# Performance work log

Hardware: AMD Instinct MI355X
Metric: run time of the kernel (lower is better)

## Reference

```python
import jax, jax.numpy as jnp
import numpy as np

L, B, H, D, S, FF = 24, 4, 16, 512, 4096, 2048
HD = D // H
POS = 2048  # current kv_cache_len (write position)
EPS = 1e-5
SCALE = 1.0 / np.sqrt(HD)


def layer_norm(x, w, b):
    m = jnp.mean(x, axis=-1, keepdims=True)
    v = jnp.mean(jnp.square(x - m), axis=-1, keepdims=True)
    return (x - m) * jax.lax.rsqrt(v + EPS) * w + b


def setup_inputs() -> dict:
    key = jax.random.key(0)
    ks = jax.random.split(key, 12)
    f = lambda k, shape: jax.random.normal(k, shape, dtype=jnp.float32) * 0.02
    # decode mask: positions [0, POS] are attendable (index_fill_ sets POS True)
    attn_mask = jnp.broadcast_to(jnp.arange(S) <= POS, (B, H, 1, S))
    return {
        "x": jax.random.normal(ks[0], (B, 1, D), dtype=jnp.float32),
        "k_cache": jax.random.normal(ks[1], (L, B, H, S, HD), dtype=jnp.float32),
        "v_cache": jax.random.normal(ks[2], (L, B, H, S, HD), dtype=jnp.float32),
        "attn_mask": attn_mask,
        "qkv_w": f(ks[3], (L, 3 * D, D)),
        "qkv_b": f(ks[4], (L, 3 * D)),
        "out_w": f(ks[5], (L, D, D)),
        "out_b": f(ks[6], (L, D)),
        "mlp_w1": f(ks[7], (L, FF, D)),
        "mlp_b1": f(ks[8], (L, FF)),
        "mlp_w2": f(ks[9], (L, D, FF)),
        "mlp_b2": f(ks[10], (L, D)),
        "norm_w1": jnp.ones((L, D), jnp.float32),
        "norm_b1": jnp.zeros((L, D), jnp.float32),
        "norm_w2": jnp.ones((L, D), jnp.float32),
        "norm_b2": jnp.zeros((L, D), jnp.float32),
        "kv_cache_len": POS,
    }


def reference(x, k_cache, v_cache, attn_mask, qkv_w, qkv_b, out_w, out_b,
              mlp_w1, mlp_b1, mlp_w2, mlp_b2, norm_w1, norm_b1, norm_w2,
              norm_b2, kv_cache_len):
    pos = kv_cache_len

    def block(h, p):
        kc0, vc0, qw, qb, ow, ob, w1, b1, w2, b2, nw1, nb1, nw2, nb2 = p
        qkv = h @ qw.T + qb                      # [B,1,3D]
        q, k, v = jnp.split(qkv, 3, axis=-1)
        q = q.reshape(B, 1, H, HD).transpose(0, 2, 1, 3)   # [B,H,1,HD]
        k = k.reshape(B, 1, H, HD).transpose(0, 2, 1, 3)
        v = v.reshape(B, 1, H, HD).transpose(0, 2, 1, 3)
        # in-place cache update at write position (index_copy_ on dim 2)
        kc = kc0.at[:, :, pos, :].set(k[:, :, 0, :])       # [B,H,S,HD]
        vc = vc0.at[:, :, pos, :].set(v[:, :, 0, :])
        scores = jnp.einsum('bhqd,bhkd->bhqk', q, kc) * SCALE
        scores = jnp.where(attn_mask, scores, -1e9)
        attn = jnp.einsum('bhqk,bhkd->bhqd', jax.nn.softmax(scores, axis=-1), vc)
        attn = attn.transpose(0, 2, 1, 3).reshape(B, 1, D)
        attn = attn @ ow.T + ob
        h = layer_norm(h + attn, nw1, nb1)
        mlp = jax.nn.relu(h @ w1.T + b1) @ w2.T + b2
        h = layer_norm(h + mlp, nw2, nb2)
        return h, None

    xs = (k_cache, v_cache, qkv_w, qkv_b, out_w, out_b, mlp_w1, mlp_b1,
          mlp_w2, mlp_b2, norm_w1, norm_b1, norm_w2, norm_b2)
    out, _ = jax.lax.scan(block, x, xs)
    return out
```

## Files before the change

### kernel.cpp

```cpp
#include <hip/hip_runtime.h>
#include <hip/hip_cooperative_groups.h>

namespace cg = cooperative_groups;


#define DEV __device__ __forceinline__

static constexpr int LNUM = 24;
static constexpr int B = 4;
static constexpr int H = 16;
static constexpr int D = 512;
static constexpr int S = 4096;
static constexpr int FF = 2048;
static constexpr int HD = 32;
static constexpr int NCH = 9;
static constexpr float EPS = 1e-5f;
static constexpr float SCALE = 0.17677669529663687f;

DEV float waveReduceSum(float v) {
#pragma unroll
    for (int o = 32; o > 0; o >>= 1) v += __shfl_xor(v, o);
    return v;
}
DEV float waveReduceMax(float v) {
#pragma unroll
    for (int o = 32; o > 0; o >>= 1) v = fmaxf(v, __shfl_xor(v, o));
    return v;
}
DEV float blockReduceSum(float v, volatile float* red) {
    v = waveReduceSum(v);
    __syncthreads();
    if ((threadIdx.x & 63) == 0) red[threadIdx.x >> 6] = v;
    __syncthreads();
    return red[0] + red[1] + red[2] + red[3];
}
DEV float blockReduceMax(float v, volatile float* red) {
    v = waveReduceMax(v);
    __syncthreads();
    if ((threadIdx.x & 63) == 0) red[threadIdx.x >> 6] = v;
    __syncthreads();
    return fmaxf(fmaxf(red[0], red[1]), fmaxf(red[2], red[3]));
}

struct Params {
    const float *x, *kc, *vc;
    const float *qkvw, *qkvb, *outw, *outb, *w1, *b1, *w2, *b2;
    const float *nw1, *nb1, *nw2, *nb2;
    const int* posp;
    float *qkvbuf, *part, *t1, *m1, *sbuf, *out;
};

__global__ __launch_bounds__(256, 2) void mega(Params p) {
    cg::grid_group grid = cg::this_grid();
    const int blk = blockIdx.x;
    const int tid = threadIdx.x;
    const int w = tid >> 6;
    const int lane = tid & 63;
    const int pos = p.posp[0];

    __shared__ float SM[6160];
    float* red = SM + 6152;

    for (int l = 0; l < LNUM; ++l) {
        const float* hsrc = (l == 0) ? p.x : p.sbuf;
        const bool aln = (l > 0);
        const float* pnw = p.nw2 + (aln ? (size_t)(l - 1) * 512 : 0);
        const float* pnb = p.nb2 + (aln ? (size_t)(l - 1) * 512 : 0);
        const float* qwL = p.qkvw + (size_t)l * 1536 * 512;
        const float* qbL = p.qkvb + (size_t)l * 1536;
        const float* kcL = p.kc + (size_t)l * 8388608;
        const float* vcL = p.vc + (size_t)l * 8388608;
        const float* owL = p.outw + (size_t)l * 512 * 512;
        const float* obL = p.outb + (size_t)l * 512;
        const float* w1L = p.w1 + (size_t)l * 2048 * 512;
        const float* b1L = p.b1 + (size_t)l * 2048;
        const float* w2L = p.w2 + (size_t)l * 512 * 2048;
        const float* b2L = p.b2 + (size_t)l * 512;
        const float* n1w = p.nw1 + (size_t)l * 512;
        const float* n1b = p.nb1 + (size_t)l * 512;

        {
            const float4* s4 = (const float4*)hsrc;
            float4* m4 = (float4*)SM;
            m4[tid] = s4[tid];
            m4[tid + 256] = s4[tid + 256];
            __syncthreads();
            float4* h4 = (float4*)(SM + (w << 9));
            float4 aa = h4[lane], bb = h4[lane + 64];
            float s = aa.x + aa.y + aa.z + aa.w + bb.x + bb.y + bb.z + bb.w;
            float s2 = aa.x * aa.x + aa.y * aa.y + aa.z * aa.z + aa.w * aa.w
                     + bb.x * bb.x + bb.y * bb.y + bb.z * bb.z + bb.w * bb.w;
            s = waveReduceSum(s);
            s2 = waveReduceSum(s2);
            float mean = s * (1.f / 512.f);
            float rs = rsqrtf(s2 * (1.f / 512.f) - mean * mean + EPS);
            if (aln) {
                const float4* gw4 = (const float4*)pnw;
                const float4* gb4 = (const float4*)pnb;
                float4 gw = gw4[lane], gb = gb4[lane];
                aa.x = (aa.x - mean) * rs * gw.x + gb.x;
                aa.y = (aa.y - mean) * rs * gw.y + gb.y;
                aa.z = (aa.z - mean) * rs * gw.z + gb.z;
                aa.w = (aa.w - mean) * rs * gw.w + gb.w;
                h4[lane] = aa;
                gw = gw4[lane + 64]; gb = gb4[lane + 64];
                bb.x = (bb.x - mean) * rs * gw.x + gb.x;
                bb.y = (bb.y - mean) * rs * gw.y + gb.y;
                bb.z = (bb.z - mean) * rs * gw.z + gb.z;
                bb.w = (bb.w - mean) * rs * gw.w + gb.w;
                h4[lane + 64] = bb;
            }
            __syncthreads();
            const int r = (blk << 2) + w;
            if (r < 1536) {
                const float4* wr4 = (const float4*)(qwL + (size_t)r * 512);
                float4 wA = wr4[lane], wB = wr4[lane + 64];
                float acc[4];
#pragma unroll
                for (int b = 0; b < 4; ++b) {
                    const float4* hb4 = (const float4*)(SM + (b << 9));
                    float4 hA = hb4[lane], hB = hb4[lane + 64];
                    float a = wA.x * hA.x + wA.y * hA.y + wA.z * hA.z + wA.w * hA.w
                            + wB.x * hB.x + wB.y * hB.y + wB.z * hB.z + wB.w * hB.w;
                    acc[b] = waveReduceSum(a);
                }
                if (lane == 0) {
                    float bias = qbL[r];
                    float sc = (r < 512) ? SCALE : 1.f;
#pragma unroll
                    for (int b = 0; b < 4; ++b)
                        p.qkvbuf[b * 1536 + r] = (acc[b] + bias) * sc;
                }
            }
        }
        grid.sync();

        {
            const int c = blk & 7, bh = blk >> 3;
            const int b = bh >> 4, h = bh & 15;
            float* qs = SM;
            float* es = SM + 32;
            float* op = SM + 288;
            float* sn = SM + 560;
            if (tid < 32) qs[tid] = p.qkvbuf[b * 1536 + h * 32 + tid];
            __syncthreads();
            const int pp = (c << 8) + tid;
            const bool act = pp < pos;
            const float4* kp = (const float4*)(kcL + ((size_t)bh * 4096 + pp) * 32);
            float sc = 0.f;
#pragma unroll
            for (int i = 0; i < 8; ++i) {
                float4 kv = kp[i];
                sc += qs[4 * i] * kv.x + qs[4 * i + 1] * kv.y
                    + qs[4 * i + 2] * kv.z + qs[4 * i + 3] * kv.w;
            }
            float score = act ? sc : -1e30f;
            float smax = score;
            float snew = 0.f;
            if (c == 7 && tid == 0) {
                const float* kn = p.qkvbuf + b * 1536 + 512 + h * 32;
                for (int j = 0; j < 32; ++j) snew += qs[j] * kn[j];
                smax = fmaxf(smax, snew);
            }
            float m = blockReduceMax(smax, red);
            if (tid == 0) sn[0] = (c == 7) ? expf(snew - m) : 0.f;
            float e = act ? expf(score - m) : 0.f;
            es[tid] = e;
            float lsum = blockReduceSum(e, red) + sn[0];
            const int d = tid & 31, g = tid >> 5;
            float acc = 0.f;
            const float* vp = vcL + ((size_t)bh * 4096 + (c << 8) + (g << 5)) * 32 + d;
#pragma unroll 8
            for (int i = 0; i < 32; ++i) acc += es[(g << 5) + i] * vp[(size_t)i * 32];
            if (g == 0) acc += sn[0] * p.qkvbuf[b * 1536 + 1024 + h * 32 + d];
            op[g * 33 + d] = acc;
            __syncthreads();
            if (tid < 32) {
                float o = 0.f;
#pragma unroll
                for (int gg = 0; gg < 8; ++gg) o += op[gg * 33 + tid];
                float* pt = p.part + (size_t)((bh << 3) + c) * 34;
                pt[2 + tid] = o;
                if (tid == 0) { pt[0] = m; pt[1] = lsum; }
            }
        }
        grid.sync();

        {
            const float4* s4 = (const float4*)hsrc;
            float4* m4 = (float4*)SM;
            m4[tid] = s4[tid];
            m4[tid + 256] = s4[tid + 256];
            __syncthreads();
            float4* h4 = (float4*)(SM + (w << 9));
            float4 aa = h4[lane], bb = h4[lane + 64];
            float s = aa.x + aa.y + aa.z + aa.w + bb.x + bb.y + bb.z + bb.w;
            float s2 = aa.x * aa.x + aa.y * aa.y + aa.z * aa.z + aa.w * aa.w
                     + bb.x * bb.x + bb.y * bb.y + bb.z * bb.z + bb.w * bb.w;
            s = waveReduceSum(s);
            s2 = waveReduceSum(s2);
            float mean = s * (1.f / 512.f);
            float rs = rsqrtf(s2 * (1.f / 512.f) - mean * mean + EPS);
            if (tid < 64) {
                const float* pt = p.part + (size_t)(tid << 3) * 34;
                float mh = -1e30f;
#pragma unroll
                for (int cc = 0; cc < 8; ++cc) mh = fmaxf(mh, pt[cc * 34]);
                float ssum = 0.f;
#pragma unroll
                for (int cc = 0; cc < 8; ++cc) ssum += pt[cc * 34 + 1] * expf(pt[cc * 34] - mh);
                SM[2048 + tid] = mh;
                SM[2112 + tid] = ssum;
            }
            __syncthreads();
#pragma unroll
            for (int k = 0; k < 8; ++k) {
                int idx = tid + (k << 8);
                int b = idx >> 9, e = idx & 511, hh = e >> 5, dd = e & 31;
                int bh = (b << 4) + hh;
                const float* pt = p.part + (size_t)(bh << 3) * 34;
                float mh = SM[2048 + bh];
                float inv = 1.f / SM[2112 + bh];
                float o = 0.f;
#pragma unroll
                for (int cc = 0; cc < 8; ++cc) o += pt[cc * 34 + 2 + dd] * expf(pt[cc * 34] - mh);
                SM[2176 + idx] = o * inv;
            }
            __syncthreads();
            const int dd = blk;
            const float4* wr4 = (const float4*)(owL + (size_t)dd * 512);
            float4 wA = wr4[lane], wB = wr4[lane + 64];
            const float4* a4 = (const float4*)(SM + 2176 + (w << 9));
            float4 hA = a4[lane], hB = a4[lane + 64];
            float acc = wA.x * hA.x + wA.y * hA.y + wA.z * hA.z + wA.w * hA.w
                      + wB.x * hB.x + wB.y * hB.y + wB.z * hB.z + wB.w * hB.w;
            acc = waveReduceSum(acc);
            if (lane == 0) {
                float hv = SM[(w << 9) + dd];
                if (aln) hv = (hv - mean) * rs * pnw[dd] + pnb[dd];
                p.t1[(w << 9) + dd] = hv + acc + obL[dd];
            }
        }
        grid.sync();

        {
            const float4* s4 = (const float4*)p.t1;
            float4* m4 = (float4*)SM;
            m4[tid] = s4[tid];
            m4[tid + 256] = s4[tid + 256];
            __syncthreads();
            float4* h4 = (float4*)(SM + (w << 9));
            float4 aa = h4[lane], bb = h4[lane + 64];
            float s = aa.x + aa.y + aa.z + aa.w + bb.x + bb.y + bb.z + bb.w;
            float s2 = aa.x * aa.x + aa.y * aa.y + aa.z * aa.z + aa.w * aa.w
                     + bb.x * bb.x + bb.y * bb.y + bb.z * bb.z + bb.w * bb.w;
            s = waveReduceSum(s);
            s2 = waveReduceSum(s2);
            float mean = s * (1.f / 512.f);
            float rs = rsqrtf(s2 * (1.f / 512.f) - mean * mean + EPS);
            {
                const float4* gw4 = (const float4*)n1w;
                const float4* gb4 = (const float4*)n1b;
                float4 gw = gw4[lane], gb = gb4[lane];
                aa.x = (aa.x - mean) * rs * gw.x + gb.x;
                aa.y = (aa.y - mean) * rs * gw.y + gb.y;
                aa.z = (aa.z - mean) * rs * gw.z + gb.z;
                aa.w = (aa.w - mean) * rs * gw.w + gb.w;
                h4[lane] = aa;
                gw = gw4[lane + 64]; gb = gb4[lane + 64];
                bb.x = (bb.x - mean) * rs * gw.x + gb.x;
                bb.y = (bb.y - mean) * rs * gw.y + gb.y;
                bb.z = (bb.z - mean) * rs * gw.z + gb.z;
                bb.w = (bb.w - mean) * rs * gw.w + gb.w;
                h4[lane + 64] = bb;
            }
            __syncthreads();
            const int r = (blk << 2) + w;
            const float4* wr4 = (const float4*)(w1L + (size_t)r * 512);
            float4 wA = wr4[lane], wB = wr4[lane + 64];
            float acc[4];
#pragma unroll
            for (int b = 0; b < 4; ++b) {
                const float4* hb4 = (const float4*)(SM + (b << 9));
                float4 hA = hb4[lane], hB = hb4[lane + 64];
                float a = wA.x * hA.x + wA.y * hA.y + wA.z * hA.z + wA.w * hA.w
                        + wB.x * hB.x + wB.y * hB.y + wB.z * hB.z + wB.w * hB.w;
                acc[b] = waveReduceSum(a);
            }
            if (lane == 0) {
                float bv = b1L[r];
#pragma unroll
                for (int b = 0; b < 4; ++b)
                    p.m1[(b << 11) + r] = fmaxf(acc[b] + bv, 0.f);
            }
        }
        grid.sync();

        {
            const float4* t4 = (const float4*)p.t1;
            float4* tB = (float4*)(SM + 4096);
            tB[tid] = t4[tid];
            tB[tid + 256] = t4[tid + 256];
            __syncthreads();
            const float4* h4 = (const float4*)(SM + 4096 + (w << 9));
            float4 aa = h4[lane], bb = h4[lane + 64];
            float s = aa.x + aa.y + aa.z + aa.w + bb.x + bb.y + bb.z + bb.w;
            float s2 = aa.x * aa.x + aa.y * aa.y + aa.z * aa.z + aa.w * aa.w
                     + bb.x * bb.x + bb.y * bb.y + bb.z * bb.z + bb.w * bb.w;
            s = waveReduceSum(s);
            s2 = waveReduceSum(s2);
            float mean = s * (1.f / 512.f);
            float rs = rsqrtf(s2 * (1.f / 512.f) - mean * mean + EPS);
            const int dd = blk;
            const float4* wr4 = (const float4*)(w2L + (size_t)dd * 2048);
            float acc = 0.f;
#pragma unroll
            for (int half = 0; half < 2; ++half) {
                __syncthreads();
#pragma unroll
                for (int i = 0; i < 4; ++i) {
                    int idx = tid + (i << 8);
                    int b = idx >> 8;
                    int f = idx & 255;
                    ((float4*)SM)[idx] =
                        ((const float4*)(p.m1 + (b << 11) + (half << 10)))[f];
                }
                __syncthreads();
                const float4* mb4 = (const float4*)SM + (w << 8);
#pragma unroll
                for (int i = 0; i < 4; ++i) {
                    float4 q = wr4[(half << 8) + (i << 6) + lane];
                    float4 mm = mb4[(i << 6) + lane];
                    acc += q.x * mm.x + q.y * mm.y + q.z * mm.z + q.w * mm.w;
                }
            }
            acc = waveReduceSum(acc);
            if (lane == 0) {
                float tv = SM[4096 + (w << 9) + dd];
                float hv = (tv - mean) * rs * n1w[dd] + n1b[dd];
                p.sbuf[(w << 9) + dd] = hv + acc + b2L[dd];
            }
        }
        grid.sync();
    }

    if (blk < 4) {
        const int b = blk;
        const float* nw = p.nw2 + 23 * 512;
        const float* nb = p.nb2 + 23 * 512;
        float a0 = p.sbuf[(b << 9) + tid];
        float a1 = p.sbuf[(b << 9) + 256 + tid];
        float s = blockReduceSum(a0 + a1, red);
        float s2 = blockReduceSum(a0 * a0 + a1 * a1, red);
        float mean = s * (1.f / 512.f);
        float rs = rsqrtf(s2 * (1.f / 512.f) - mean * mean + EPS);
        p.out[(b << 9) + tid] = (a0 - mean) * rs * nw[tid] + nb[tid];
        p.out[(b << 9) + 256 + tid] = (a1 - mean) * rs * nw[tid + 256] + nb[tid + 256];
    }
}

__global__ __launch_bounds__(256) void k_qkv(
    const float* __restrict__ hsrc, int apply_ln,
    const float* __restrict__ nw, const float* __restrict__ nb,
    const float* __restrict__ w, const float* __restrict__ bias,
    float* __restrict__ qkv)
{
    const int lane = threadIdx.x & 63;
    const int wid = (blockIdx.x << 2) + (threadIdx.x >> 6);
    const int b = wid / 1536;
    const int r = wid - b * 1536;
    const float* hb = hsrc + (b << 9);
    const int k0 = lane << 3;
    float4 h0 = *(const float4*)(hb + k0);
    float4 h1 = *(const float4*)(hb + k0 + 4);
    float hv[8] = {h0.x, h0.y, h0.z, h0.w, h1.x, h1.y, h1.z, h1.w};
    if (apply_ln) {
        float s = 0.f, s2 = 0.f;
#pragma unroll
        for (int j = 0; j < 8; ++j) { s += hv[j]; s2 += hv[j] * hv[j]; }
        s = waveReduceSum(s);
        s2 = waveReduceSum(s2);
        float mean = s * (1.f / 512.f);
        float rs = rsqrtf(s2 * (1.f / 512.f) - mean * mean + EPS);
        float4 nw0 = *(const float4*)(nw + k0);
        float4 nw1 = *(const float4*)(nw + k0 + 4);
        float4 nb0 = *(const float4*)(nb + k0);
        float4 nb1 = *(const float4*)(nb + k0 + 4);
        float nwv[8] = {nw0.x, nw0.y, nw0.z, nw0.w, nw1.x, nw1.y, nw1.z, nw1.w};
        float nbv[8] = {nb0.x, nb0.y, nb0.z, nb0.w, nb1.x, nb1.y, nb1.z, nb1.w};
#pragma unroll
        for (int j = 0; j < 8; ++j) hv[j] = (hv[j] - mean) * rs * nwv[j] + nbv[j];
    }
    const float* wr = w + (size_t)r * 512 + k0;
    float4 w0 = *(const float4*)(wr);
    float4 w1 = *(const float4*)(wr + 4);
    float acc = w0.x * hv[0] + w0.y * hv[1] + w0.z * hv[2] + w0.w * hv[3]
              + w1.x * hv[4] + w1.y * hv[5] + w1.z * hv[6] + w1.w * hv[7];
    acc = waveReduceSum(acc);
    if (lane == 0) {
        float v = acc + bias[r];
        if (r < 512) v *= SCALE;
        qkv[b * 1536 + r] = v;
    }
}

__global__ __launch_bounds__(256) void k_attn(
    const float* __restrict__ kc, const float* __restrict__ vc,
    const float* __restrict__ qkv, float* __restrict__ part,
    const int* __restrict__ posp)
{
    const int tid = threadIdx.x;
    const int c = blockIdx.x % NCH;
    const int bh = blockIdx.x / NCH;
    const int b = bh >> 4, h = bh & 15;
    const int pos = posp[0];
    __shared__ float qs[32];
    __shared__ float es[256];
    __shared__ float red[4];
    __shared__ float op[8][33];
    if (tid < 32) qs[tid] = qkv[b * 1536 + h * 32 + tid];
    __syncthreads();
    float score = -1e30f;
    bool act = false;
    if (c < 8) {
        int p = c * 256 + tid;
        act = (p < pos);
        const float4* kp = (const float4*)(kc + ((size_t)bh * S + p) * HD);
        float s = 0.f;
#pragma unroll
        for (int i = 0; i < 8; ++i) {
            float4 kv = kp[i];
            s += qs[4 * i] * kv.x + qs[4 * i + 1] * kv.y + qs[4 * i + 2] * kv.z + qs[4 * i + 3] * kv.w;
        }
        if (act) score = s;
    } else if (tid == 0) {
        act = true;
        const float* kp = qkv + b * 1536 + 512 + h * 32;
        float s = 0.f;
#pragma unroll
        for (int j = 0; j < 32; ++j) s += qs[j] * kp[j];
        score = s;
    }
    float m = blockReduceMax(score, red);
    float e = act ? expf(score - m) : 0.f;
    es[tid] = e;
    float l = blockReduceSum(e, red);
    const int d = tid & 31, g = tid >> 5;
    float acc = 0.f;
    if (c < 8) {
        const float* vp = vc + ((size_t)bh * S + c * 256 + g * 32) * HD + d;
#pragma unroll 8
        for (int i = 0; i < 32; ++i) acc += es[g * 32 + i] * vp[(size_t)i * HD];
    } else if (g == 0) {
        acc = es[0] * qkv[b * 1536 + 1024 + h * 32 + d];
    }
    op[g][d] = acc;
    __syncthreads();
    if (tid < 32) {
        float o = 0.f;
#pragma unroll
        for (int gg = 0; gg < 8; ++gg) o += op[gg][tid];
        float* pp = part + (size_t)(bh * NCH + c) * 34;
        pp[2 + tid] = o;
        if (tid == 0) { pp[0] = m; pp[1] = l; }
    }
}

__global__ __launch_bounds__(256) void k_outproj(
    const float* __restrict__ part,
    const float* __restrict__ ow, const float* __restrict__ ob,
    const float* __restrict__ hsrc, int apply_ln,
    const float* __restrict__ nw, const float* __restrict__ nb,
    float* __restrict__ t1)
{
    const int tid = threadIdx.x;
    const int b = blockIdx.x >> 5;
    const int oc = blockIdx.x & 31;
    __shared__ float attn_s[512];
    __shared__ float hln[512];
    __shared__ float mh[16], sh[16];
    __shared__ float red[4];
    if (tid < 16) {
        const float* pp = part + (size_t)(b * 16 + tid) * NCH * 34;
        float m = -1e30f;
        for (int c = 0; c < NCH; ++c) m = fmaxf(m, pp[c * 34]);
        float ss = 0.f;
        for (int c = 0; c < NCH; ++c) ss += pp[c * 34 + 1] * expf(pp[c * 34] - m);
        mh[tid] = m;
        sh[tid] = ss;
    }
    __syncthreads();
#pragma unroll
    for (int e = tid; e < 512; e += 256) {
        int h = e >> 5, d = e & 31;
        const float* pp = part + (size_t)(b * 16 + h) * NCH * 34;
        float o = 0.f;
        for (int c = 0; c < NCH; ++c) o += pp[c * 34 + 2 + d] * expf(pp[c * 34] - mh[h]);
        attn_s[e] = o / sh[h];
    }
    float a0 = hsrc[(b << 9) + tid], a1 = hsrc[(b << 9) + 256 + tid];
    if (apply_ln) {
        float s = blockReduceSum(a0 + a1, red);
        float s2 = blockReduceSum(a0 * a0 + a1 * a1, red);
        float mean = s * (1.f / 512.f);
        float rs = rsqrtf(s2 * (1.f / 512.f) - mean * mean + EPS);
        hln[tid] = (a0 - mean) * rs * nw[tid] + nb[tid];
        hln[tid + 256] = (a1 - mean) * rs * nw[tid + 256] + nb[tid + 256];
    } else {
        hln[tid] = a0;
        hln[tid + 256] = a1;
    }
    __syncthreads();
    const int w = tid >> 6, lane = tid & 63, k0 = lane << 3;
#pragma unroll
    for (int oi = 0; oi < 4; ++oi) {
        int dd = (oc << 4) + (w << 2) + oi;
        const float4* wp = (const float4*)(ow + (size_t)dd * 512 + k0);
        float4 w0 = wp[0], w1 = wp[1];
        float acc = w0.x * attn_s[k0] + w0.y * attn_s[k0 + 1] + w0.z * attn_s[k0 + 2] + w0.w * attn_s[k0 + 3]
                  + w1.x * attn_s[k0 + 4] + w1.y * attn_s[k0 + 5] + w1.z * attn_s[k0 + 6] + w1.w * attn_s[k0 + 7];
        acc = waveReduceSum(acc);
        if (lane == 0) t1[(b << 9) + dd] = hln[dd] + acc + ob[dd];
    }
}

__global__ __launch_bounds__(256) void k_mlp1(
    const float* __restrict__ t1,
    const float* __restrict__ nw, const float* __restrict__ nb,
    const float* __restrict__ w1, const float* __restrict__ b1,
    float* __restrict__ m1)
{
    const int tid = threadIdx.x;
    const int b = blockIdx.x >> 7;
    const int oc = blockIdx.x & 127;
    __shared__ float hln[512];
    __shared__ float red[4];
    float a0 = t1[(b << 9) + tid], a1 = t1[(b << 9) + 256 + tid];
    float s = blockReduceSum(a0 + a1, red);
    float s2 = blockReduceSum(a0 * a0 + a1 * a1, red);
    float mean = s * (1.f / 512.f);
    float rs = rsqrtf(s2 * (1.f / 512.f) - mean * mean + EPS);
    hln[tid] = (a0 - mean) * rs * nw[tid] + nb[tid];
    hln[tid + 256] = (a1 - mean) * rs * nw[tid + 256] + nb[tid + 256];
    __syncthreads();
    const int w = tid >> 6, lane = tid & 63, k0 = lane << 3;
#pragma unroll
    for (int oi = 0; oi < 4; ++oi) {
        int r = (oc << 4) + (w << 2) + oi;
        const float4* wp = (const float4*)(w1 + (size_t)r * 512 + k0);
        float4 w0 = wp[0], w1v = wp[1];
        float acc = w0.x * hln[k0] + w0.y * hln[k0 + 1] + w0.z * hln[k0 + 2] + w0.w * hln[k0 + 3]
                  + w1v.x * hln[k0 + 4] + w1v.y * hln[k0 + 5] + w1v.z * hln[k0 + 6] + w1v.w * hln[k0 + 7];
        acc = waveReduceSum(acc);
        if (lane == 0) m1[(b << 11) + r] = fmaxf(acc + b1[r], 0.f);
    }
}

__global__ __launch_bounds__(256) void k_mlp2(
    const float* __restrict__ m1, const float* __restrict__ t1,
    const float* __restrict__ nw, const float* __restrict__ nb,
    const float* __restrict__ w2, const float* __restrict__ b2,
    float* __restrict__ sout)
{
    const int tid = threadIdx.x;
    const int b = blockIdx.x >> 7;
    const int oc = blockIdx.x & 127;
    __shared__ float ms[2048];
    __shared__ float red[4];
#pragma unroll
    for (int i = 0; i < 8; ++i) ms[tid + (i << 8)] = m1[(b << 11) + tid + (i << 8)];
    float a0 = t1[(b << 9) + tid], a1 = t1[(b << 9) + 256 + tid];
    float s = blockReduceSum(a0 + a1, red);
    float s2 = blockReduceSum(a0 * a0 + a1 * a1, red);
    float mean = s * (1.f / 512.f);
    float rs = rsqrtf(s2 * (1.f / 512.f) - mean * mean + EPS);
    const int w = tid >> 6, lane = tid & 63;
    const int dd = (oc << 2) + w;
    const float4* wp = (const float4*)(w2 + (size_t)dd * 2048);
    float acc = 0.f;
#pragma unroll
    for (int i = 0; i < 8; ++i) {
        int idx = (i << 6) + lane;
        float4 q = wp[idx];
        int k = idx << 2;
        acc += q.x * ms[k] + q.y * ms[k + 1] + q.z * ms[k + 2] + q.w * ms[k + 3];
    }
    acc = waveReduceSum(acc);
    if (lane == 0) {
        float td = t1[(b << 9) + dd];
        float hd = (td - mean) * rs * nw[dd] + nb[dd];
        sout[(b << 9) + dd] = hd + acc + b2[dd];
    }
}

__global__ __launch_bounds__(256) void k_finalln(
    const float* __restrict__ sbuf,
    const float* __restrict__ nw, const float* __restrict__ nb,
    float* __restrict__ out)
{
    const int b = blockIdx.x, tid = threadIdx.x;
    __shared__ float red[4];
    float a0 = sbuf[(b << 9) + tid], a1 = sbuf[(b << 9) + 256 + tid];
    float s = blockReduceSum(a0 + a1, red);
    float s2 = blockReduceSum(a0 * a0 + a1 * a1, red);
    float mean = s * (1.f / 512.f);
    float rs = rsqrtf(s2 * (1.f / 512.f) - mean * mean + EPS);
    out[(b << 9) + tid] = (a0 - mean) * rs * nw[tid] + nb[tid];
    out[(b << 9) + 256 + tid] = (a1 - mean) * rs * nw[tid + 256] + nb[tid + 256];
}

extern "C" void kernel_launch(void* const* d_in, const int* in_sizes, int n_in,
                              void* d_out, int out_size, void* d_ws, size_t ws_size,
                              hipStream_t stream)
{
    const float* x    = (const float*)d_in[0];
    const float* kc   = (const float*)d_in[1];
    const float* vc   = (const float*)d_in[2];
    const float* qkvw = (const float*)d_in[4];
    const float* qkvb = (const float*)d_in[5];
    const float* outw = (const float*)d_in[6];
    const float* outb = (const float*)d_in[7];
    const float* w1   = (const float*)d_in[8];
    const float* b1   = (const float*)d_in[9];
    const float* w2   = (const float*)d_in[10];
    const float* b2   = (const float*)d_in[11];
    const float* nw1  = (const float*)d_in[12];
    const float* nb1  = (const float*)d_in[13];
    const float* nw2  = (const float*)d_in[14];
    const float* nb2  = (const float*)d_in[15];
    const int*   posp = (const int*)d_in[16];

    int dev = 0, cu = 0, nb = 0;
    hipGetDevice(&dev);
    hipDeviceGetAttribute(&cu, hipDeviceAttributeMultiprocessorCount, dev);
    hipOccupancyMaxActiveBlocksPerMultiprocessor(&nb, (const void*)mega, 256, 0);
    const bool coop_ok = ((long)nb * cu >= 512);

    float* ws = (float*)d_ws;

    if (coop_ok) {
        Params prm;
        prm.x = x; prm.kc = kc; prm.vc = vc;
        prm.qkvw = qkvw; prm.qkvb = qkvb; prm.outw = outw; prm.outb = outb;
        prm.w1 = w1; prm.b1 = b1; prm.w2 = w2; prm.b2 = b2;
        prm.nw1 = nw1; prm.nb1 = nb1; prm.nw2 = nw2; prm.nb2 = nb2;
        prm.posp = posp;
        prm.qkvbuf = ws;
        prm.part   = prm.qkvbuf + 6144;
        prm.t1     = prm.part + 17408;
        prm.m1     = prm.t1 + 2048;
        prm.sbuf   = prm.m1 + 8192;
        prm.out    = (float*)d_out;
        void* args[] = { &prm };
        hipLaunchCooperativeKernel(reinterpret_cast<const void*>(&mega),
                                   dim3(512), dim3(256), args, 0, stream);
        return;
    }

    float* qkvbuf = ws;
    float* part   = qkvbuf + 6144;
    float* t1     = part + 19584;
    float* m1     = t1 + 2048;
    float* sbuf   = m1 + 8192;
    const size_t kvLayerStride = (size_t)B * H * S * HD;

    for (int l = 0; l < LNUM; ++l) {
        const float* hsrc = (l == 0) ? x : sbuf;
        const int aln = (l > 0) ? 1 : 0;
        const float* pnw = (l > 0) ? (nw2 + (size_t)(l - 1) * 512) : nullptr;
        const float* pnb = (l > 0) ? (nb2 + (size_t)(l - 1) * 512) : nullptr;

        k_qkv<<<1536, 256, 0, stream>>>(hsrc, aln, pnw, pnb,
                                        qkvw + (size_t)l * 1536 * 512,
                                        qkvb + (size_t)l * 1536, qkvbuf);
        k_attn<<<B * H * NCH, 256, 0, stream>>>(kc + (size_t)l * kvLayerStride,
                                                vc + (size_t)l * kvLayerStride,
                                                qkvbuf, part, posp);
        k_outproj<<<B * 32, 256, 0, stream>>>(part,
                                              outw + (size_t)l * 512 * 512,
                                              outb + (size_t)l * 512,
                                              hsrc, aln, pnw, pnb, t1);
        k_mlp1<<<B * 128, 256, 0, stream>>>(t1,
                                            nw1 + (size_t)l * 512, nb1 + (size_t)l * 512,
                                            w1 + (size_t)l * FF * D, b1 + (size_t)l * FF, m1);
        k_mlp2<<<B * 128, 256, 0, stream>>>(m1, t1,
                                            nw1 + (size_t)l * 512, nb1 + (size_t)l * 512,
                                            w2 + (size_t)l * D * FF, b2 + (size_t)l * 512, sbuf);
    }
    k_finalln<<<B, 256, 0, stream>>>(sbuf, nw2 + 23 * 512, nb2 + 23 * 512, (float*)d_out);
}
```

Measured before the change: 844.5 us.

## Replace grid.sync with split arrive/wait atomic barrier and prefetch weights before waits

Swaps the cooperative-groups grid sync for a monotonic atomic counter barrier split into an arrive phase and a wait phase. Each stage now loads the data that does not depend on the previous stage (K/V cache rows, out-proj, W1 and W2 rows, next layer's QKV rows, LN params) before waiting, so those global loads overlap barrier latency. This raises register pressure, since for example 32 V values and 8 W2 float4s are held per thread, and it relies on hand-written acquire/release fencing being correct. A memset of the counter is added before each launch.

```diff
diff --git a/kernel.cpp b/kernel.cpp
--- a/kernel.cpp
+++ b/kernel.cpp
@@ -1,7 +1,4 @@
 #include <hip/hip_runtime.h>
-#include <hip/hip_cooperative_groups.h>
-
-namespace cg = cooperative_groups;
 
 
 #define DEV __device__ __forceinline__
@@ -14,6 +11,7 @@
 static constexpr int FF = 2048;
 static constexpr int HD = 32;
 static constexpr int NCH = 9;
+static constexpr int NBLK = 512;
 static constexpr float EPS = 1e-5f;
 static constexpr float SCALE = 0.17677669529663687f;
 
@@ -40,6 +38,20 @@
     if ((threadIdx.x & 63) == 0) red[threadIdx.x >> 6] = v;
     __syncthreads();
     return fmaxf(fmaxf(red[0], red[1]), fmaxf(red[2], red[3]));
+}
+
+DEV void gbar_arrive(unsigned* ctr) {
+    __syncthreads();
+    if (threadIdx.x == 0)
+        __hip_atomic_fetch_add(ctr, 1u, __ATOMIC_RELEASE, __HIP_MEMORY_SCOPE_AGENT);
+}
+DEV void gbar_wait(unsigned* ctr, unsigned target) {
+    if (threadIdx.x == 0) {
+        while (__hip_atomic_load(ctr, __ATOMIC_RELAXED, __HIP_MEMORY_SCOPE_AGENT) < target)
+            __builtin_amdgcn_s_sleep(1);
+        __builtin_amdgcn_fence(__ATOMIC_ACQUIRE, "agent");
+    }
+    __syncthreads();
 }
 
 struct Params {
@@ -48,25 +60,34 @@
     const float *nw1, *nb1, *nw2, *nb2;
     const int* posp;
     float *qkvbuf, *part, *t1, *m1, *sbuf, *out;
+    unsigned* bar;
 };
 
 __global__ __launch_bounds__(256, 2) void mega(Params p) {
-    cg::grid_group grid = cg::this_grid();
     const int blk = blockIdx.x;
     const int tid = threadIdx.x;
     const int w = tid >> 6;
     const int lane = tid & 63;
     const int pos = p.posp[0];
+    unsigned* ctr = p.bar;
+    unsigned nbar = 0;
 
     __shared__ float SM[6160];
     float* red = SM + 6152;
+
+    const int r1 = (blk << 2) + w;
+
+    float4 wA, wB;
+    if (r1 < 1536) {
+        const float4* wr4 = (const float4*)(p.qkvw + (size_t)r1 * 512);
+        wA = wr4[lane]; wB = wr4[lane + 64];
+    }
 
     for (int l = 0; l < LNUM; ++l) {
         const float* hsrc = (l == 0) ? p.x : p.sbuf;
         const bool aln = (l > 0);
         const float* pnw = p.nw2 + (aln ? (size_t)(l - 1) * 512 : 0);
         const float* pnb = p.nb2 + (aln ? (size_t)(l - 1) * 512 : 0);
-        const float* qwL = p.qkvw + (size_t)l * 1536 * 512;
         const float* qbL = p.qkvb + (size_t)l * 1536;
         const float* kcL = p.kc + (size_t)l * 8388608;
         const float* vcL = p.vc + (size_t)l * 8388608;
@@ -80,16 +101,17 @@
         const float* n1b = p.nb1 + (size_t)l * 512;
 
         {
+            if (l) gbar_wait(ctr, nbar * NBLK);
             const float4* s4 = (const float4*)hsrc;
+            float4 hr0 = s4[tid], hr1 = s4[tid + 256];
             float4* m4 = (float4*)SM;
-            m4[tid] = s4[tid];
-            m4[tid + 256] = s4[tid + 256];
+            m4[tid] = hr0; m4[tid + 256] = hr1;
             __syncthreads();
             float4* h4 = (float4*)(SM + (w << 9));
-            float4 aa = h4[lane], bb = h4[lane + 64];
-            float s = aa.x + aa.y + aa.z + aa.w + bb.x + bb.y + bb.z + bb.w;
+            float4 aa = h4[lane], bbv = h4[lane + 64];
+            float s = aa.x + aa.y + aa.z + aa.w + bbv.x + bbv.y + bbv.z + bbv.w;
             float s2 = aa.x * aa.x + aa.y * aa.y + aa.z * aa.z + aa.w * aa.w
-                     + bb.x * bb.x + bb.y * bb.y + bb.z * bb.z + bb.w * bb.w;
+                     + bbv.x * bbv.x + bbv.y * bbv.y + bbv.z * bbv.z + bbv.w * bbv.w;
             s = waveReduceSum(s);
             s2 = waveReduceSum(s2);
             float mean = s * (1.f / 512.f);
@@ -104,17 +126,14 @@
                 aa.w = (aa.w - mean) * rs * gw.w + gb.w;
                 h4[lane] = aa;
                 gw = gw4[lane + 64]; gb = gb4[lane + 64];
-                bb.x = (bb.x - mean) * rs * gw.x + gb.x;
-                bb.y = (bb.y - mean) * rs * gw.y + gb.y;
-                bb.z = (bb.z - mean) * rs * gw.z + gb.z;
-                bb.w = (bb.w - mean) * rs * gw.w + gb.w;
-                h4[lane + 64] = bb;
-            }
-            __syncthreads();
-            const int r = (blk << 2) + w;
-            if (r < 1536) {
-                const float4* wr4 = (const float4*)(qwL + (size_t)r * 512);
-                float4 wA = wr4[lane], wB = wr4[lane + 64];
+                bbv.x = (bbv.x - mean) * rs * gw.x + gb.x;
+                bbv.y = (bbv.y - mean) * rs * gw.y + gb.y;
+                bbv.z = (bbv.z - mean) * rs * gw.z + gb.z;
+                bbv.w = (bbv.w - mean) * rs * gw.w + gb.w;
+                h4[lane + 64] = bbv;
+            }
+            __syncthreads();
+            if (r1 < 1536) {
                 float acc[4];
 #pragma unroll
                 for (int b = 0; b < 4; ++b) {
@@ -125,40 +144,49 @@
                     acc[b] = waveReduceSum(a);
                 }
                 if (lane == 0) {
-                    float bias = qbL[r];
-                    float sc = (r < 512) ? SCALE : 1.f;
+                    float bias = qbL[r1];
+                    float sc = (r1 < 512) ? SCALE : 1.f;
 #pragma unroll
                     for (int b = 0; b < 4; ++b)
-                        p.qkvbuf[b * 1536 + r] = (acc[b] + bias) * sc;
+                        p.qkvbuf[b * 1536 + r1] = (acc[b] + bias) * sc;
                 }
             }
+            gbar_arrive(ctr); ++nbar;
         }
-        grid.sync();
 
         {
             const int c = blk & 7, bh = blk >> 3;
-            const int b = bh >> 4, h = bh & 15;
+            const int bb2 = bh >> 4, hh2 = bh & 15;
+            const int pp2 = (c << 8) + tid;
+            float4 kpre[8];
+            {
+                const float4* kp = (const float4*)(kcL + ((size_t)bh * 4096 + pp2) * 32);
+#pragma unroll
+                for (int i = 0; i < 8; ++i) kpre[i] = kp[i];
+            }
+            float vpre[32];
+            {
+                const float* vp = vcL + ((size_t)bh * 4096 + (c << 8) + ((tid >> 5) << 5)) * 32 + (tid & 31);
+#pragma unroll
+                for (int i = 0; i < 32; ++i) vpre[i] = vp[(size_t)i * 32];
+            }
+            gbar_wait(ctr, nbar * NBLK);
             float* qs = SM;
             float* es = SM + 32;
             float* op = SM + 288;
             float* sn = SM + 560;
-            if (tid < 32) qs[tid] = p.qkvbuf[b * 1536 + h * 32 + tid];
-            __syncthreads();
-            const int pp = (c << 8) + tid;
-            const bool act = pp < pos;
-            const float4* kp = (const float4*)(kcL + ((size_t)bh * 4096 + pp) * 32);
+            if (tid < 32) qs[tid] = p.qkvbuf[bb2 * 1536 + (hh2 << 5) + tid];
+            __syncthreads();
             float sc = 0.f;
 #pragma unroll
-            for (int i = 0; i < 8; ++i) {
-                float4 kv = kp[i];
-                sc += qs[4 * i] * kv.x + qs[4 * i + 1] * kv.y
-                    + qs[4 * i + 2] * kv.z + qs[4 * i + 3] * kv.w;
-            }
+            for (int i = 0; i < 8; ++i)
+                sc += qs[4 * i] * kpre[i].x + qs[4 * i + 1] * kpre[i].y
+                    + qs[4 * i + 2] * kpre[i].z + qs[4 * i + 3] * kpre[i].w;
+            const bool act = pp2 < pos;
             float score = act ? sc : -1e30f;
-            float smax = score;
-            float snew = 0.f;
+            float smax = score, snew = 0.f;
             if (c == 7 && tid == 0) {
-                const float* kn = p.qkvbuf + b * 1536 + 512 + h * 32;
+                const float* kn = p.qkvbuf + bb2 * 1536 + 512 + (hh2 << 5);
                 for (int j = 0; j < 32; ++j) snew += qs[j] * kn[j];
                 smax = fmaxf(smax, snew);
             }
@@ -169,10 +197,9 @@
             float lsum = blockReduceSum(e, red) + sn[0];
             const int d = tid & 31, g = tid >> 5;
             float acc = 0.f;
-            const float* vp = vcL + ((size_t)bh * 4096 + (c << 8) + (g << 5)) * 32 + d;
-#pragma unroll 8
-            for (int i = 0; i < 32; ++i) acc += es[(g << 5) + i] * vp[(size_t)i * 32];
-            if (g == 0) acc += sn[0] * p.qkvbuf[b * 1536 + 1024 + h * 32 + d];
+#pragma unroll
+            for (int i = 0; i < 32; ++i) acc += es[(g << 5) + i] * vpre[i];
+            if (g == 0) acc += sn[0] * p.qkvbuf[bb2 * 1536 + 1024 + (hh2 << 5) + d];
             op[g * 33 + d] = acc;
             __syncthreads();
             if (tid < 32) {
@@ -183,20 +210,26 @@
                 pt[2 + tid] = o;
                 if (tid == 0) { pt[0] = m; pt[1] = lsum; }
             }
+            gbar_arrive(ctr); ++nbar;
         }
-        grid.sync();
 
         {
+            float4 oA, oB;
+            {
+                const float4* wr4 = (const float4*)(owL + (size_t)blk * 512);
+                oA = wr4[lane]; oB = wr4[lane + 64];
+            }
             const float4* s4 = (const float4*)hsrc;
+            float4 hr0 = s4[tid], hr1 = s4[tid + 256];
+            gbar_wait(ctr, nbar * NBLK);
             float4* m4 = (float4*)SM;
-            m4[tid] = s4[tid];
-            m4[tid + 256] = s4[tid + 256];
+            m4[tid] = hr0; m4[tid + 256] = hr1;
             __syncthreads();
             float4* h4 = (float4*)(SM + (w << 9));
-            float4 aa = h4[lane], bb = h4[lane + 64];
-            float s = aa.x + aa.y + aa.z + aa.w + bb.x + bb.y + bb.z + bb.w;
+            float4 aa = h4[lane], bbv = h4[lane + 64];
+            float s = aa.x + aa.y + aa.z + aa.w + bbv.x + bbv.y + bbv.z + bbv.w;
             float s2 = aa.x * aa.x + aa.y * aa.y + aa.z * aa.z + aa.w * aa.w
-                     + bb.x * bb.x + bb.y * bb.y + bb.z * bb.z + bb.w * bb.w;
+                     + bbv.x * bbv.x + bbv.y * bbv.y + bbv.z * bbv.z + bbv.w * bbv.w;
             s = waveReduceSum(s);
             s2 = waveReduceSum(s2);
             float mean = s * (1.f / 512.f);
@@ -227,92 +260,95 @@
                 SM[2176 + idx] = o * inv;
             }
             __syncthreads();
-            const int dd = blk;
-            const float4* wr4 = (const float4*)(owL + (size_t)dd * 512);
-            float4 wA = wr4[lane], wB = wr4[lane + 64];
             const float4* a4 = (const float4*)(SM + 2176 + (w << 9));
             float4 hA = a4[lane], hB = a4[lane + 64];
-            float acc = wA.x * hA.x + wA.y * hA.y + wA.z * hA.z + wA.w * hA.w
-                      + wB.x * hB.x + wB.y * hB.y + wB.z * hB.z + wB.w * hB.w;
+            float acc = oA.x * hA.x + oA.y * hA.y + oA.z * hA.z + oA.w * hA.w
+                      + oB.x * hB.x + oB.y * hB.y + oB.z * hB.z + oB.w * hB.w;
             acc = waveReduceSum(acc);
             if (lane == 0) {
-                float hv = SM[(w << 9) + dd];
-                if (aln) hv = (hv - mean) * rs * pnw[dd] + pnb[dd];
-                p.t1[(w << 9) + dd] = hv + acc + obL[dd];
-            }
+                float hv = SM[(w << 9) + blk];
+                if (aln) hv = (hv - mean) * rs * pnw[blk] + pnb[blk];
+                p.t1[(w << 9) + blk] = hv + acc + obL[blk];
+            }
+            gbar_arrive(ctr); ++nbar;
         }
-        grid.sync();
 
         {
-            const float4* s4 = (const float4*)p.t1;
+            float4 w1A, w1B, g0, g1, gb0, gb1;
+            {
+                const float4* wr4 = (const float4*)(w1L + (size_t)r1 * 512);
+                w1A = wr4[lane]; w1B = wr4[lane + 64];
+                const float4* gw4 = (const float4*)n1w;
+                const float4* gbb = (const float4*)n1b;
+                g0 = gw4[lane]; g1 = gw4[lane + 64];
+                gb0 = gbb[lane]; gb1 = gbb[lane + 64];
+            }
+            gbar_wait(ctr, nbar * NBLK);
+            const float4* t4 = (const float4*)p.t1;
+            float4 tr0 = t4[tid], tr1 = t4[tid + 256];
             float4* m4 = (float4*)SM;
-            m4[tid] = s4[tid];
-            m4[tid + 256] = s4[tid + 256];
+            m4[tid] = tr0; m4[tid + 256] = tr1;
             __syncthreads();
             float4* h4 = (float4*)(SM + (w << 9));
-            float4 aa = h4[lane], bb = h4[lane + 64];
-            float s = aa.x + aa.y + aa.z + aa.w + bb.x + bb.y + bb.z + bb.w;
+            float4 aa = h4[lane], bbv = h4[lane + 64];
+            float s = aa.x + aa.y + aa.z + aa.w + bbv.x + bbv.y + bbv.z + bbv.w;
             float s2 = aa.x * aa.x + aa.y * aa.y + aa.z * aa.z + aa.w * aa.w
-                     + bb.x * bb.x + bb.y * bb.y + bb.z * bb.z + bb.w * bb.w;
+                     + bbv.x * bbv.x + bbv.y * bbv.y + bbv.z * bbv.z + bbv.w * bbv.w;
             s = waveReduceSum(s);
             s2 = waveReduceSum(s2);
             float mean = s * (1.f / 512.f);
             float rs = rsqrtf(s2 * (1.f / 512.f) - mean * mean + EPS);
-            {
-                const float4* gw4 = (const float4*)n1w;
-                const float4* gb4 = (const float4*)n1b;
-                float4 gw = gw4[lane], gb = gb4[lane];
-                aa.x = (aa.x - mean) * rs * gw.x + gb.x;
-                aa.y = (aa.y - mean) * rs * gw.y + gb.y;
-                aa.z = (aa.z - mean) * rs * gw.z + gb.z;
-                aa.w = (aa.w - mean) * rs * gw.w + gb.w;
-                h4[lane] = aa;
-                gw = gw4[lane + 64]; gb = gb4[lane + 64];
-                bb.x = (bb.x - mean) * rs * gw.x + gb.x;
-                bb.y = (bb.y - mean) * rs * gw.y + gb.y;
-                bb.z = (bb.z - mean) * rs * gw.z + gb.z;
-                bb.w = (bb.w - mean) * rs * gw.w + gb.w;
-                h4[lane + 64] = bb;
-            }
-            __syncthreads();
-            const int r = (blk << 2) + w;
-            const float4* wr4 = (const float4*)(w1L + (size_t)r * 512);
-            float4 wA = wr4[lane], wB = wr4[lane + 64];
+            aa.x = (aa.x - mean) * rs * g0.x + gb0.x;
+            aa.y = (aa.y - mean) * rs * g0.y + gb0.y;
+            aa.z = (aa.z - mean) * rs * g0.z + gb0.z;
+            aa.w = (aa.w - mean) * rs * g0.w + gb0.w;
+            h4[lane] = aa;
+            bbv.x = (bbv.x - mean) * rs * g1.x + gb1.x;
+            bbv.y = (bbv.y - mean) * rs * g1.y + gb1.y;
+            bbv.z = (bbv.z - mean) * rs * g1.z + gb1.z;
+            bbv.w = (bbv.w - mean) * rs * g1.w + gb1.w;
+            h4[lane + 64] = bbv;
+            __syncthreads();
             float acc[4];
 #pragma unroll
             for (int b = 0; b < 4; ++b) {
                 const float4* hb4 = (const float4*)(SM + (b << 9));
                 float4 hA = hb4[lane], hB = hb4[lane + 64];
-                float a = wA.x * hA.x + wA.y * hA.y + wA.z * hA.z + wA.w * hA.w
-                        + wB.x * hB.x + wB.y * hB.y + wB.z * hB.z + wB.w * hB.w;
+                float a = w1A.x * hA.x + w1A.y * hA.y + w1A.z * hA.z + w1A.w * hA.w
+                        + w1B.x * hB.x + w1B.y * hB.y + w1B.z * hB.z + w1B.w * hB.w;
                 acc[b] = waveReduceSum(a);
             }
             if (lane == 0) {
-                float bv = b1L[r];
+                float bv = b1L[r1];
 #pragma unroll
                 for (int b = 0; b < 4; ++b)
-                    p.m1[(b << 11) + r] = fmaxf(acc[b] + bv, 0.f);
-            }
+                    p.m1[(b << 11) + r1] = fmaxf(acc[b] + bv, 0.f);
+            }
+            gbar_arrive(ctr); ++nbar;
         }
-        grid.sync();
 
         {
+            float4 w2pre[8];
+            {
+                const float4* wr4 = (const float4*)(w2L + (size_t)blk * 2048);
+#pragma unroll
+                for (int i = 0; i < 8; ++i) w2pre[i] = wr4[(i << 6) + lane];
+            }
             const float4* t4 = (const float4*)p.t1;
+            float4 tr0 = t4[tid], tr1 = t4[tid + 256];
+            gbar_wait(ctr, nbar * NBLK);
             float4* tB = (float4*)(SM + 4096);
-            tB[tid] = t4[tid];
-            tB[tid + 256] = t4[tid + 256];
+            tB[tid] = tr0; tB[tid + 256] = tr1;
             __syncthreads();
             const float4* h4 = (const float4*)(SM + 4096 + (w << 9));
-            float4 aa = h4[lane], bb = h4[lane + 64];
-            float s = aa.x + aa.y + aa.z + aa.w + bb.x + bb.y + bb.z + bb.w;
+            float4 aa = h4[lane], bbv = h4[lane + 64];
+            float s = aa.x + aa.y + aa.z + aa.w + bbv.x + bbv.y + bbv.z + bbv.w;
             float s2 = aa.x * aa.x + aa.y * aa.y + aa.z * aa.z + aa.w * aa.w
-                     + bb.x * bb.x + bb.y * bb.y + bb.z * bb.z + bb.w * bb.w;
+                     + bbv.x * bbv.x + bbv.y * bbv.y + bbv.z * bbv.z + bbv.w * bbv.w;
             s = waveReduceSum(s);
             s2 = waveReduceSum(s2);
             float mean = s * (1.f / 512.f);
             float rs = rsqrtf(s2 * (1.f / 512.f) - mean * mean + EPS);
-            const int dd = blk;
-            const float4* wr4 = (const float4*)(w2L + (size_t)dd * 2048);
             float acc = 0.f;
 #pragma unroll
             for (int half = 0; half < 2; ++half) {
@@ -320,30 +356,35 @@
 #pragma unroll
                 for (int i = 0; i < 4; ++i) {
                     int idx = tid + (i << 8);
-                    int b = idx >> 8;
-                    int f = idx & 255;
+                    int bb3 = idx >> 8, f = idx & 255;
                     ((float4*)SM)[idx] =
-                        ((const float4*)(p.m1 + (b << 11) + (half << 10)))[f];
+                        ((const float4*)(p.m1 + (bb3 << 11) + (half << 10)))[f];
                 }
                 __syncthreads();
                 const float4* mb4 = (const float4*)SM + (w << 8);
 #pragma unroll
                 for (int i = 0; i < 4; ++i) {
-                    float4 q = wr4[(half << 8) + (i << 6) + lane];
+                    float4 q = w2pre[(half << 2) + i];
                     float4 mm = mb4[(i << 6) + lane];
                     acc += q.x * mm.x + q.y * mm.y + q.z * mm.z + q.w * mm.w;
                 }
             }
             acc = waveReduceSum(acc);
             if (lane == 0) {
-                float tv = SM[4096 + (w << 9) + dd];
-                float hv = (tv - mean) * rs * n1w[dd] + n1b[dd];
-                p.sbuf[(w << 9) + dd] = hv + acc + b2L[dd];
-            }
+                float tv = SM[4096 + (w << 9) + blk];
+                float hv = (tv - mean) * rs * n1w[blk] + n1b[blk];
+                p.sbuf[(w << 9) + blk] = hv + acc + b2L[blk];
+            }
+            gbar_arrive(ctr); ++nbar;
         }
-        grid.sync();
-    }
-
+
+        if (l + 1 < LNUM && r1 < 1536) {
+            const float4* wr4 = (const float4*)(p.qkvw + (size_t)(l + 1) * 1536 * 512 + (size_t)r1 * 512);
+            wA = wr4[lane]; wB = wr4[lane + 64];
+        }
+    }
+
+    gbar_wait(ctr, nbar * NBLK);
     if (blk < 4) {
         const int b = blk;
         const float* nw = p.nw2 + 23 * 512;
@@ -634,7 +675,7 @@
     hipGetDevice(&dev);
     hipDeviceGetAttribute(&cu, hipDeviceAttributeMultiprocessorCount, dev);
     hipOccupancyMaxActiveBlocksPerMultiprocessor(&nb, (const void*)mega, 256, 0);
-    const bool coop_ok = ((long)nb * cu >= 512);
+    const bool coop_ok = ((long)nb * cu >= NBLK);
 
     float* ws = (float*)d_ws;
 
@@ -651,9 +692,11 @@
         prm.m1     = prm.t1 + 2048;
         prm.sbuf   = prm.m1 + 8192;
         prm.out    = (float*)d_out;
+        prm.bar    = (unsigned*)(ws + 35840);
+        hipMemsetAsync(prm.bar, 0, 64, stream);
         void* args[] = { &prm };
         hipLaunchCooperativeKernel(reinterpret_cast<const void*>(&mega),
-                                   dim3(512), dim3(256), args, 0, stream);
+                                   dim3(NBLK), dim3(256), args, 0, stream);
         return;
     }
 
```

Result: no change. 843.1 us (-0.2%).
